# Kernel optimization log

Measured on AMD Instinct MI355X. Metric: run time of the kernel, lower is better.

Reference implementation:

```python
import jax, jax.numpy as jnp
import numpy as np

N = 8192   # nodes in each graph (N1 must equal N2: V is built from x1)
D = 512    # output_dim


def setup_inputs() -> dict:
    key = jax.random.key(0)
    k1, k2, kq, kk, kv = jax.random.split(key, 5)
    std = 1.0 / np.sqrt(D)
    return {
        "x1": jax.random.normal(k1, (N, D), dtype=jnp.float32),
        "x2": jax.random.normal(k2, (N, D), dtype=jnp.float32),
        "q": jax.random.uniform(kq, (D, D), dtype=jnp.float32, minval=-std, maxval=std),
        "k": jax.random.uniform(kk, (D, D), dtype=jnp.float32, minval=-std, maxval=std),
        "v": jax.random.uniform(kv, (D, D), dtype=jnp.float32, minval=-std, maxval=std),
    }


def reference(x1, x2, q, k, v):
    Q = x1 @ q                       # [N, D]
    V = x1 @ v                       # [N, D]  (note: V from x1, as in the original)
    K = x2 @ k                       # [N, D]
    e = jax.nn.leaky_relu(Q @ K.T, negative_slope=0.01)  # [N, N]
    attention = jax.nn.softmax(e, axis=-1)
    return attention @ V             # [N, D]
```

## Files before the change

### kernel.cpp

```cpp
#include <hip/hip_runtime.h>
#include <hip/hip_bf16.h>

typedef unsigned short u16;
typedef unsigned int u32;
typedef float floatx4 __attribute__((ext_vector_type(4)));
typedef _Float16 f16x8 __attribute__((ext_vector_type(8)));

#define NN 8192
#define DD 512
#define NPARTS 4
#define JCHUNK 2048
#define RB_PER_PART 64

__device__ __forceinline__ u16 f2h(float f) {
    _Float16 h = (_Float16)f;
    return __builtin_bit_cast(u16, h);
}
__device__ __forceinline__ float h2f(u16 u) {
    _Float16 h = __builtin_bit_cast(_Float16, u);
    return (float)h;
}

__device__ __forceinline__ void async16(const u16* g, u16* l) {
    __builtin_amdgcn_global_load_lds(
        (const __attribute__((address_space(1))) u32*)g,
        (__attribute__((address_space(3))) u32*)l, 16, 0, 0);
}

__global__ __launch_bounds__(256, 2)
void proj_kernel(const float* __restrict__ x1, const float* __restrict__ x2,
                 const float* __restrict__ qw, const float* __restrict__ kw,
                 const float* __restrict__ vw,
                 u16* __restrict__ Qf, u16* __restrict__ Kf, u16* __restrict__ VT)
{
    const int which = blockIdx.z;
    const float* A = (which == 1) ? x2 : x1;
    const float* W = (which == 0) ? qw : (which == 1 ? kw : vw);

    __shared__ u16 Ash[128 * 40];
    __shared__ u16 Wsh[128 * 40];

    const int tid  = threadIdx.x;
    const int lane = tid & 63;
    const int wave = tid >> 6;
    const int l15  = lane & 15;
    const int quad = lane >> 4;
    const int wm   = (wave & 1) * 64;
    const int wn   = (wave >> 1) * 64;
    const int m0   = blockIdx.x * 128;
    const int n0   = blockIdx.y * 128;

    floatx4 acc[4][4] = {};

    for (int k0 = 0; k0 < DD; k0 += 32) {
        __syncthreads();
        {
            const int cg = (tid & 7) * 4;
            for (int i = 0; i < 4; i++) {
                const int row = (tid >> 3) + i * 32;
                float4 f = *(const float4*)&A[(size_t)(m0 + row) * DD + k0 + cg];
                uint2 p;
                p.x = ((unsigned)f2h(f.y) << 16) | f2h(f.x);
                p.y = ((unsigned)f2h(f.w) << 16) | f2h(f.z);
                *(uint2*)&Ash[row * 40 + cg] = p;
            }
        }
        {
            const int kr = tid & 31;
            const int g  = tid >> 5;
            for (int i = 0; i < 4; i++) {
                const int n = (g + i * 8) * 4;
                float4 f = *(const float4*)&W[(size_t)(k0 + kr) * DD + n0 + n];
                Wsh[(n + 0) * 40 + kr] = f2h(f.x);
                Wsh[(n + 1) * 40 + kr] = f2h(f.y);
                Wsh[(n + 2) * 40 + kr] = f2h(f.z);
                Wsh[(n + 3) * 40 + kr] = f2h(f.w);
            }
        }
        __syncthreads();

        f16x8 af[4], bf[4];
        for (int mi = 0; mi < 4; mi++)
            af[mi] = *(const f16x8*)&Ash[(wm + mi * 16 + l15) * 40 + quad * 8];
        for (int ni = 0; ni < 4; ni++)
            bf[ni] = *(const f16x8*)&Wsh[(wn + ni * 16 + l15) * 40 + quad * 8];
        for (int mi = 0; mi < 4; mi++)
            for (int ni = 0; ni < 4; ni++)
                acc[mi][ni] = __builtin_amdgcn_mfma_f32_16x16x32_f16(
                    af[mi], bf[ni], acc[mi][ni], 0, 0, 0);
    }

    for (int mi = 0; mi < 4; mi++)
        for (int ni = 0; ni < 4; ni++)
            for (int r = 0; r < 4; r++) {
                const int row = m0 + wm + mi * 16 + quad * 4 + r;
                const int col = n0 + wn + ni * 16 + l15;
                const u16 hv = f2h(acc[mi][ni][r]);
                if (which == 0)      Qf[(size_t)row * DD + col] = hv;
                else if (which == 1) Kf[(size_t)row * DD + col] = hv;
                else                 VT[(size_t)col * NN + row] = hv;
            }
}

__global__ __launch_bounds__(512, 2)
void attn_kernel(const u16* __restrict__ Qf, const u16* __restrict__ Kf,
                 const u16* __restrict__ VT,
                 u16* __restrict__ Opart, float* __restrict__ Mp,
                 float* __restrict__ Lp, int* __restrict__ cnt)
{
    const int tid  = threadIdx.x;
    const int lane = tid & 63;
    const int wave = tid >> 6;
    const int w3   = wave & 3;
    const int wsel = wave >> 2;
    const int l15  = lane & 15;
    const int quad = lane >> 4;

    __shared__ u16 KV[6][8192];
    __shared__ u16 Ps[8][16 * 68];
    __shared__ int sPart, sRb;

    if (tid == 0) {
        u32 xcd;
        asm volatile("s_getreg_b32 %0, hwreg(HW_REG_XCC_ID)" : "=s"(xcd));
        xcd &= 3;
        int part = -1, rb = 0;
        for (int t = 0; t < 4; t++) {
            const int p = (xcd + t) & 3;
            const int idx = atomicAdd(&cnt[p], 1);
            if (idx < RB_PER_PART) { part = p; rb = idx; break; }
        }
        sPart = part; sRb = rb;
    }
    __syncthreads();
    const int part = sPart;
    const int rb   = sRb;
    if (part < 0) return;

    const int q0 = rb * 128 + wave * 16;

    f16x8 qf[16];
    for (int kk = 0; kk < 16; kk++)
        qf[kk] = *(const f16x8*)&Qf[(size_t)(q0 + l15) * DD + kk * 32 + quad * 8];

    floatx4 o[32] = {};
    float m_run[4], l_run[4];
    for (int r = 0; r < 4; r++) { m_run[r] = -1e30f; l_run[r] = 0.f; }

    const int j_begin = part * JCHUNK;
    const int j_end   = j_begin + JCHUNK;

    const int krow4  = lane >> 4;
    const int kpos16 = lane & 15;
    const int vrs    = lane >> 3;
    const int vch    = (lane & 7) ^ vrs;

    int kOff[4], vOff[4];
    for (int i = 0; i < 4; i++) {
        const int c    = w3 * 4 + i;
        const int krow = c * 4 + krow4;
        kOff[i] = krow * DD + (kpos16 ^ (krow & 7)) * 8;
        vOff[i] = (c * 8 + vrs) * NN + vch * 8;
    }

    auto stageK = [&](int dq, int j0, int slot) {
        const u16* b = Kf + (size_t)j0 * DD + dq * 128;
        u16* d = &KV[slot][w3 * 2048];
        async16(b + kOff[0], d);
        async16(b + kOff[1], d + 512);
        async16(b + kOff[2], d + 1024);
        async16(b + kOff[3], d + 1536);
        __builtin_amdgcn_sched_barrier(0);
    };
    auto stageV = [&](int dq, int j0, int slot) {
        const u16* b = VT + (size_t)dq * 128 * NN + j0;
        u16* d = &KV[slot][w3 * 2048];
        async16(b + vOff[0], d);
        async16(b + vOff[1], d + 512);
        async16(b + vOff[2], d + 1024);
        async16(b + vOff[3], d + 1536);
        __builtin_amdgcn_sched_barrier(0);
    };

    auto qkQ = [&](int rg, int dq, floatx4* s) {
        __builtin_amdgcn_s_setprio(1);
        for (int k8 = 0; k8 < 4; k8++)
            for (int nt = 0; nt < 4; nt++) {
                const int row = nt * 16 + l15;
                const int ch  = (k8 * 4 + quad) ^ (l15 & 7);
                f16x8 b = *(const f16x8*)&KV[rg][row * 128 + ch * 8];
                s[nt] = __builtin_amdgcn_mfma_f32_16x16x32_f16(qf[dq * 4 + k8], b, s[nt], 0, 0, 0);
            }
        __builtin_amdgcn_s_setprio(0);
    };
    auto pvQ = [&](int rg, int dq) {
        f16x8 pf0 = *(const f16x8*)&Ps[wave][l15 * 68 + quad * 8];
        f16x8 pf1 = *(const f16x8*)&Ps[wave][l15 * 68 + 32 + quad * 8];
        __builtin_amdgcn_s_setprio(1);
        for (int t = 0; t < 8; t++) {
            const int row = t * 16 + l15;
            const int c0  = quad ^ (l15 & 7);
            const int c1  = (4 + quad) ^ (l15 & 7);
            f16x8 b0 = *(const f16x8*)&KV[rg][row * 64 + c0 * 8];
            f16x8 b1 = *(const f16x8*)&KV[rg][row * 64 + c1 * 8];
            o[dq * 8 + t] = __builtin_amdgcn_mfma_f32_16x16x32_f16(pf0, b0, o[dq * 8 + t], 0, 0, 0);
            o[dq * 8 + t] = __builtin_amdgcn_mfma_f32_16x16x32_f16(pf1, b1, o[dq * 8 + t], 0, 0, 0);
        }
        __builtin_amdgcn_s_setprio(0);
    };

    auto pbar = [&]() {
        asm volatile("s_waitcnt vmcnt(4)" ::: "memory");
        asm volatile("s_barrier" ::: "memory");
    };
    auto wrap6 = [](int x) { return x >= 6 ? x - 6 : x; };

    if (wsel == 0) stageK(0, j_begin, 0); else stageK(1, j_begin, 1);
    if (wsel == 0) stageK(2, j_begin, 2); else stageK(3, j_begin, 3);
    asm volatile("s_waitcnt vmcnt(0)" ::: "memory");
    asm volatile("s_barrier" ::: "memory");

    int sc = 4;

    for (int j0 = j_begin; j0 < j_end; j0 += 64) {
        const int jn = (j0 + 64 < j_end) ? j0 + 64 : j_begin;
        floatx4 s[4] = {};
        int sA, sB, cA, cB;

        sA = sc; sB = sc + 1; cA = wrap6(sc + 2); cB = cA + 1; sc = cA;
        if (wsel == 0) stageV(0, j0, sA); else stageV(1, j0, sB);
        qkQ(cA, 0, s);
        qkQ(cB, 1, s);
        pbar();

        sA = sc; sB = sc + 1; cA = wrap6(sc + 2); cB = cA + 1; sc = cA;
        if (wsel == 0) stageV(2, j0, sA); else stageV(3, j0, sB);
        qkQ(cA, 2, s);
        qkQ(cB, 3, s);

        for (int nt = 0; nt < 4; nt++)
            for (int r = 0; r < 4; r++) {
                float x = s[nt][r];
                s[nt][r] = x >= 0.f ? x : 0.01f * x;
            }
        float mt[4];
        for (int r = 0; r < 4; r++)
            mt[r] = fmaxf(fmaxf(s[0][r], s[1][r]), fmaxf(s[2][r], s[3][r]));
        for (int off = 1; off < 16; off <<= 1)
            for (int r = 0; r < 4; r++)
                mt[r] = fmaxf(mt[r], __shfl_xor(mt[r], off));

        float alpha[4];
        for (int r = 0; r < 4; r++) {
            const float mnew = fmaxf(m_run[r], mt[r]);
            alpha[r] = __expf(m_run[r] - mnew);
            m_run[r] = mnew;
        }
        float ls[4] = {0.f, 0.f, 0.f, 0.f};
        u16 pv[4][4];
        for (int nt = 0; nt < 4; nt++)
            for (int r = 0; r < 4; r++) {
                const float p = __expf(s[nt][r] - m_run[r]);
                ls[r] += p;
                pv[nt][r] = f2h(p);
            }
        for (int off = 1; off < 16; off <<= 1)
            for (int r = 0; r < 4; r++)
                ls[r] += __shfl_xor(ls[r], off);
        for (int r = 0; r < 4; r++)
            l_run[r] = l_run[r] * alpha[r] + ls[r];
        const bool need = (alpha[0] != 1.f) | (alpha[1] != 1.f) |
                          (alpha[2] != 1.f) | (alpha[3] != 1.f);
        if (__any(need))
            for (int i = 0; i < 32; i++)
                for (int r = 0; r < 4; r++)
                    o[i][r] *= alpha[r];

        for (int nt = 0; nt < 4; nt++)
            for (int r = 0; r < 4; r++)
                Ps[wave][(quad * 4 + r) * 68 + nt * 16 + l15] = pv[nt][r];
        asm volatile("s_waitcnt lgkmcnt(0)" ::: "memory");

        pbar();

        sA = sc; sB = sc + 1; cA = wrap6(sc + 2); cB = cA + 1; sc = cA;
        if (wsel == 0) stageK(0, jn, sA); else stageK(1, jn, sB);
        pvQ(cA, 0);
        pvQ(cB, 1);
        pbar();

        sA = sc; sB = sc + 1; cA = wrap6(sc + 2); cB = cA + 1; sc = cA;
        if (wsel == 0) stageK(2, jn, sA); else stageK(3, jn, sB);
        pvQ(cA, 2);
        pvQ(cB, 3);
        pbar();
    }

    asm volatile("s_waitcnt vmcnt(0)" ::: "memory");

    for (int i = 0; i < 32; i++)
        for (int r = 0; r < 4; r++) {
            const int row = q0 + quad * 4 + r;
            const int col = i * 16 + l15;
            Opart[((size_t)part * NN + row) * DD + col] = f2h(o[i][r]);
        }
    if (l15 == 0)
        for (int r = 0; r < 4; r++) {
            const int row = q0 + quad * 4 + r;
            Mp[part * NN + row] = m_run[r];
            Lp[part * NN + row] = l_run[r];
        }
}

__global__ __launch_bounds__(256)
void combine_kernel(const u16* __restrict__ Opart, const float* __restrict__ Mp,
                    const float* __restrict__ Lp, float* __restrict__ out)
{
    const int t   = blockIdx.x * 256 + threadIdx.x;
    const int row = t >> 6;
    const int c0  = (t & 63) * 8;

    float m[NPARTS], l[NPARTS];
    float M = -1e30f;
    for (int p = 0; p < NPARTS; p++) {
        m[p] = Mp[p * NN + row];
        l[p] = Lp[p * NN + row];
        M = fmaxf(M, m[p]);
    }
    float w[NPARTS], L = 0.f;
    for (int p = 0; p < NPARTS; p++) { w[p] = __expf(m[p] - M); L += w[p] * l[p]; }
    const float inv = 1.f / L;

    float acc[8] = {};
    for (int p = 0; p < NPARTS; p++) {
        f16x8 v = *(const f16x8*)&Opart[((size_t)p * NN + row) * DD + c0];
        for (int j = 0; j < 8; j++)
            acc[j] += w[p] * (float)v[j];
    }
    float4 o0, o1;
    o0.x = acc[0] * inv; o0.y = acc[1] * inv; o0.z = acc[2] * inv; o0.w = acc[3] * inv;
    o1.x = acc[4] * inv; o1.y = acc[5] * inv; o1.z = acc[6] * inv; o1.w = acc[7] * inv;
    *(float4*)&out[(size_t)row * DD + c0]     = o0;
    *(float4*)&out[(size_t)row * DD + c0 + 4] = o1;
}

extern "C" void kernel_launch(void* const* d_in, const int* in_sizes, int n_in,
                              void* d_out, int out_size, void* d_ws, size_t ws_size,
                              hipStream_t stream)
{
    const float* x1 = (const float*)d_in[0];
    const float* x2 = (const float*)d_in[1];
    const float* qw = (const float*)d_in[2];
    const float* kw = (const float*)d_in[3];
    const float* vw = (const float*)d_in[4];
    float* out = (float*)d_out;

    u16* Qf = (u16*)d_ws;
    u16* Kf = Qf + (size_t)NN * DD;
    u16* VT = Kf + (size_t)NN * DD;
    u16* Opart = VT + (size_t)NN * DD;
    float* Mp = (float*)(Opart + (size_t)NPARTS * NN * DD);
    float* Lp = Mp + NPARTS * NN;
    int* cnt = (int*)(Lp + NPARTS * NN);

    hipMemsetAsync(cnt, 0, NPARTS * sizeof(int), stream);
    proj_kernel<<<dim3(64, 4, 3), 256, 0, stream>>>(x1, x2, qw, kw, vw, Qf, Kf, VT);
    attn_kernel<<<dim3(RB_PER_PART * NPARTS), 512, 0, stream>>>(Qf, Kf, VT, Opart, Mp, Lp, cnt);
    combine_kernel<<<(NN * 64) / 256, 256, 0, stream>>>(Opart, Mp, Lp, out);
}
```

Measured before the change: 372.3 us.

## Precast inputs to fp16 and double-buffer projection GEMM with async LDS loads

Adds a prep kernel that converts x1/x2 to fp16 and transposes the three weight matrices to fp16, and also zeroes the counter, replacing the memset. The projection GEMM then stages tiles with global_load_lds into double-buffered, XOR-swizzled LDS with a K-tile of 64, so the next tile's loads overlap the MFMA work. The aim is to remove the per-tile fp32 conversion and the scattered transposed LDS stores from the GEMM inner loop. In exchange it adds an extra pass over the inputs and extra workspace, and the strided transposed weight writes in prep are uncoalesced.

```diff
diff --git a/kernel.cpp b/kernel.cpp
--- a/kernel.cpp
+++ b/kernel.cpp
@@ -27,18 +27,49 @@
         (__attribute__((address_space(3))) u32*)l, 16, 0, 0);
 }
 
-__global__ __launch_bounds__(256, 2)
-void proj_kernel(const float* __restrict__ x1, const float* __restrict__ x2,
+__global__ __launch_bounds__(256)
+void prep_kernel(const float* __restrict__ x1, const float* __restrict__ x2,
                  const float* __restrict__ qw, const float* __restrict__ kw,
                  const float* __restrict__ vw,
+                 u16* __restrict__ x1h, u16* __restrict__ x2h,
+                 u16* __restrict__ qT, u16* __restrict__ kT,
+                 u16* __restrict__ vT, int* __restrict__ cnt)
+{
+    const int t = blockIdx.x * 256 + threadIdx.x;
+    const int stride = gridDim.x * 256;
+    if (t < NPARTS) cnt[t] = 0;
+
+    const int NQ = NN * DD / 4;
+    for (int i = t; i < NQ; i += stride) {
+        float4 f = ((const float4*)x1)[i];
+        ushort4 h;
+        h.x = f2h(f.x); h.y = f2h(f.y); h.z = f2h(f.z); h.w = f2h(f.w);
+        ((ushort4*)x1h)[i] = h;
+        f = ((const float4*)x2)[i];
+        h.x = f2h(f.x); h.y = f2h(f.y); h.z = f2h(f.z); h.w = f2h(f.w);
+        ((ushort4*)x2h)[i] = h;
+    }
+    const int NW = DD * DD;
+    for (int i = t; i < NW; i += stride) {
+        const int k = i >> 9, n = i & 511;
+        qT[n * DD + k] = f2h(qw[i]);
+        kT[n * DD + k] = f2h(kw[i]);
+        vT[n * DD + k] = f2h(vw[i]);
+    }
+}
+
+__global__ __launch_bounds__(256, 2)
+void proj_kernel(const u16* __restrict__ x1h, const u16* __restrict__ x2h,
+                 const u16* __restrict__ qT, const u16* __restrict__ kT,
+                 const u16* __restrict__ vT,
                  u16* __restrict__ Qf, u16* __restrict__ Kf, u16* __restrict__ VT)
 {
     const int which = blockIdx.z;
-    const float* A = (which == 1) ? x2 : x1;
-    const float* W = (which == 0) ? qw : (which == 1 ? kw : vw);
-
-    __shared__ u16 Ash[128 * 40];
-    __shared__ u16 Wsh[128 * 40];
+    const u16* A = (which == 1) ? x2h : x1h;
+    const u16* W = (which == 0) ? qT : (which == 1 ? kT : vT);
+
+    __shared__ u16 Ab[2][128 * 64];
+    __shared__ u16 Wb[2][128 * 64];
 
     const int tid  = threadIdx.x;
     const int lane = tid & 63;
@@ -50,44 +81,60 @@
     const int m0   = blockIdx.x * 128;
     const int n0   = blockIdx.y * 128;
 
+    const int vrs = lane >> 3;
+    const int vch = (lane & 7) ^ vrs;
+    int sOff[4];
+    for (int i = 0; i < 4; i++) {
+        const int c = wave * 4 + i;
+        sOff[i] = (c * 8 + vrs) * DD + vch * 8;
+    }
+
+    auto stage = [&](int buf, int k0) {
+        const u16* a = A + (size_t)m0 * DD + k0;
+        const u16* w = W + (size_t)n0 * DD + k0;
+        u16* da = &Ab[buf][wave * 2048];
+        u16* dw = &Wb[buf][wave * 2048];
+        async16(a + sOff[0], da);
+        async16(a + sOff[1], da + 512);
+        async16(a + sOff[2], da + 1024);
+        async16(a + sOff[3], da + 1536);
+        async16(w + sOff[0], dw);
+        async16(w + sOff[1], dw + 512);
+        async16(w + sOff[2], dw + 1024);
+        async16(w + sOff[3], dw + 1536);
+        __builtin_amdgcn_sched_barrier(0);
+    };
+
     floatx4 acc[4][4] = {};
 
-    for (int k0 = 0; k0 < DD; k0 += 32) {
+    stage(0, 0);
+    asm volatile("s_waitcnt vmcnt(0)" ::: "memory");
+    __syncthreads();
+
+    for (int t = 0; t < 8; t++) {
+        if (t < 7) stage((t & 1) ^ 1, (t + 1) * 64);
+        const int buf = t & 1;
+        __builtin_amdgcn_s_setprio(1);
+        for (int ks = 0; ks < 2; ks++) {
+            f16x8 af[4], bf[4];
+            for (int mi = 0; mi < 4; mi++) {
+                const int row = wm + mi * 16 + l15;
+                const int ch  = (ks * 4 + quad) ^ (l15 & 7);
+                af[mi] = *(const f16x8*)&Ab[buf][row * 64 + ch * 8];
+            }
+            for (int ni = 0; ni < 4; ni++) {
+                const int row = wn + ni * 16 + l15;
+                const int ch  = (ks * 4 + quad) ^ (l15 & 7);
+                bf[ni] = *(const f16x8*)&Wb[buf][row * 64 + ch * 8];
+            }
+            for (int mi = 0; mi < 4; mi++)
+                for (int ni = 0; ni < 4; ni++)
+                    acc[mi][ni] = __builtin_amdgcn_mfma_f32_16x16x32_f16(
+                        af[mi], bf[ni], acc[mi][ni], 0, 0, 0);
+        }
+        __builtin_amdgcn_s_setprio(0);
+        asm volatile("s_waitcnt vmcnt(0)" ::: "memory");
         __syncthreads();
-        {
-            const int cg = (tid & 7) * 4;
-            for (int i = 0; i < 4; i++) {
-                const int row = (tid >> 3) + i * 32;
-                float4 f = *(const float4*)&A[(size_t)(m0 + row) * DD + k0 + cg];
-                uint2 p;
-                p.x = ((unsigned)f2h(f.y) << 16) | f2h(f.x);
-                p.y = ((unsigned)f2h(f.w) << 16) | f2h(f.z);
-                *(uint2*)&Ash[row * 40 + cg] = p;
-            }
-        }
-        {
-            const int kr = tid & 31;
-            const int g  = tid >> 5;
-            for (int i = 0; i < 4; i++) {
-                const int n = (g + i * 8) * 4;
-                float4 f = *(const float4*)&W[(size_t)(k0 + kr) * DD + n0 + n];
-                Wsh[(n + 0) * 40 + kr] = f2h(f.x);
-                Wsh[(n + 1) * 40 + kr] = f2h(f.y);
-                Wsh[(n + 2) * 40 + kr] = f2h(f.z);
-                Wsh[(n + 3) * 40 + kr] = f2h(f.w);
-            }
-        }
-        __syncthreads();
-
-        f16x8 af[4], bf[4];
-        for (int mi = 0; mi < 4; mi++)
-            af[mi] = *(const f16x8*)&Ash[(wm + mi * 16 + l15) * 40 + quad * 8];
-        for (int ni = 0; ni < 4; ni++)
-            bf[ni] = *(const f16x8*)&Wsh[(wn + ni * 16 + l15) * 40 + quad * 8];
-        for (int mi = 0; mi < 4; mi++)
-            for (int ni = 0; ni < 4; ni++)
-                acc[mi][ni] = __builtin_amdgcn_mfma_f32_16x16x32_f16(
-                    af[mi], bf[ni], acc[mi][ni], 0, 0, 0);
     }
 
     for (int mi = 0; mi < 4; mi++)
@@ -362,9 +409,16 @@
     float* Mp = (float*)(Opart + (size_t)NPARTS * NN * DD);
     float* Lp = Mp + NPARTS * NN;
     int* cnt = (int*)(Lp + NPARTS * NN);
-
-    hipMemsetAsync(cnt, 0, NPARTS * sizeof(int), stream);
-    proj_kernel<<<dim3(64, 4, 3), 256, 0, stream>>>(x1, x2, qw, kw, vw, Qf, Kf, VT);
+    u16* x1h = (u16*)(cnt + 8);
+    u16* x2h = x1h + (size_t)NN * DD;
+    u16* qT  = x2h + (size_t)NN * DD;
+    u16* kT  = qT + DD * DD;
+    u16* vT  = kT + DD * DD;
+
+    prep_kernel<<<1024, 256, 0, stream>>>(x1, x2, qw, kw, vw,
+                                          x1h, x2h, qT, kT, vT, cnt);
+    proj_kernel<<<dim3(64, 4, 3), 256, 0, stream>>>(x1h, x2h, qT, kT, vT,
+                                                    Qf, Kf, VT);
     attn_kernel<<<dim3(RB_PER_PART * NPARTS), 512, 0, stream>>>(Qf, Kf, VT, Opart, Mp, Lp, cnt);
     combine_kernel<<<(NN * 64) / 256, 256, 0, stream>>>(Opart, Mp, Lp, out);
 }
```

After: 364.6 us. 1.02x faster.
